# Performance work log

Hardware: AMD Instinct MI355X
Metric: run time of the kernel (lower is better)

## Reference

```python
import jax, jax.numpy as jnp
import numpy as np

N, G, E, R = 32768, 2048, 1146880, 3
NIN, GIN, F, OUT = 6, 4, 64, 1


def _w(k, fan_in, fan_out):
    return (jax.random.normal(k, (fan_in, fan_out), jnp.float32) / np.sqrt(fan_in)).astype(jnp.float32)


def setup_inputs() -> dict:
    key = jax.random.key(0)
    ks = jax.random.split(key, 20)
    x = jax.random.normal(ks[0], (N, NIN), jnp.float32)
    u = jax.random.normal(ks[1], (G, GIN), jnp.float32)
    batch = jnp.sort(jax.random.randint(ks[2], (N,), 0, G))
    hyperedge_index = jax.random.randint(ks[3], (R, E), 0, N)
    batch_hyper = jnp.sort(jax.random.randint(ks[4], (E,), 0, G))
    inp = {
        "x": x, "u": u, "batch": batch,
        "hyperedge_index": hyperedge_index, "batch_hyper": batch_hyper, "r": R,
        # mlp_x: (NIN+GIN)->F->F->F
        "W1": _w(ks[5], NIN + GIN, F), "b1": jnp.zeros((F,), jnp.float32),
        "W2": _w(ks[6], F, F), "b2": jnp.zeros((F,), jnp.float32),
        "W3": _w(ks[7], F, F), "b3": jnp.zeros((F,), jnp.float32),
        # weighting matrix [F,F]
        "weight": _w(ks[8], F, F),
        # x_hat: 2F->F->F->OUT
        "V1": _w(ks[9], 2 * F, F), "c1": jnp.zeros((F,), jnp.float32),
        "V2": _w(ks[10], F, F), "c2": jnp.zeros((F,), jnp.float32),
        "V3": _w(ks[11], F, OUT), "c3": jnp.zeros((OUT,), jnp.float32),
    }
    return inp


def _segment_softmax(x, idx, num_segments):
    # torch_geometric-style softmax grouped by idx along dim 0, per feature
    seg_max = jax.ops.segment_max(x, idx, num_segments=num_segments)
    ex = jnp.exp(x - seg_max[idx])
    denom = jax.ops.segment_sum(ex, idx, num_segments=num_segments)
    return ex / denom[idx]


def reference(x, u, batch, hyperedge_index, batch_hyper, r,
              W1, b1, W2, b2, W3, b3, weight, V1, c1, V2, c2, V3, c3):
    # mlp_x on [node_feats || global_feats_of_node's_graph]
    h = jnp.concatenate([x, u[batch]], axis=1)            # [N, NIN+GIN]
    h = jnp.maximum(h @ W1 + b1, 0.0)
    h = jnp.maximum(h @ W2 + b2, 0.0)
    h = h @ W3 + b3                                        # [N, F]

    # hyperedge finding: sum the r member-node embeddings of each hyperedge
    x_hyper = jnp.zeros((hyperedge_index.shape[1], h.shape[1]), h.dtype)
    for i in range(hyperedge_index.shape[0]):              # r is small & fixed
        x_hyper = x_hyper + jnp.take(h, hyperedge_index[i], axis=0)  # [E, F]

    # weighting: segment softmax over hyperedges of the same graph
    coef = _segment_softmax(x_hyper, batch_hyper, G)       # [E, F]
    x_hyper_hat = coef * jnp.maximum(x_hyper @ weight, 0.0)

    # x_hat head
    o = jnp.concatenate([x_hyper, x_hyper_hat], axis=1)    # [E, 2F]
    o = jnp.maximum(o @ V1 + c1, 0.0)
    o = jnp.maximum(o @ V2 + c2, 0.0)
    o = jax.nn.sigmoid(o @ V3 + c3)                        # [E, OUT]
    return (o, batch_hyper)
```

## Files before the change

### kernel.cpp

```cpp
#include <hip/hip_runtime.h>
#include <math.h>

typedef short bf16x8 __attribute__((ext_vector_type(8)));
typedef float f32x4  __attribute__((ext_vector_type(4)));
typedef unsigned short u16;
typedef unsigned int   u32;

#define MFMA16 __builtin_amdgcn_mfma_f32_16x16x32_bf16

__device__ __forceinline__ u16 f2b(float x) {
    union { float f; unsigned u; } v; v.f = x;
    unsigned r = v.u + 0x7fffu + ((v.u >> 16) & 1u);
    return (u16)(r >> 16);
}
__device__ __forceinline__ u16 f2bu(float x) {
    union { float f; unsigned u; } v; v.f = x;
    return (u16)((v.u + 0x8000u) >> 16);
}
__device__ __forceinline__ float b2f(u16 h) {
    union { unsigned u; float f; } v; v.u = ((unsigned)h) << 16;
    return v.f;
}
__device__ __forceinline__ float blo(u32 w) {
    union { u32 u; float f; } v; v.u = w << 16; return v.f;
}
__device__ __forceinline__ float bhi(u32 w) {
    union { u32 u; float f; } v; v.u = w & 0xffff0000u; return v.f;
}
__device__ __forceinline__ u32 add3pack(u32 x, u32 y, u32 z) {
    union { float f; u32 u; } lo, hi;
    lo.f = blo(x) + blo(y) + blo(z);
    hi.f = bhi(x) + bhi(y) + bhi(z);
    return __builtin_amdgcn_perm(hi.u + 0x8000u, lo.u + 0x8000u, 0x07060302u);
}

#define LOG2E 1.44269504088896340736f

__global__ __launch_bounds__(256) void prep_mlp_kernel(
    const float* __restrict__ x, const float* __restrict__ u,
    const int* __restrict__ batch,
    const float* __restrict__ W1, const float* __restrict__ b1,
    const float* __restrict__ W2, const float* __restrict__ b2,
    const float* __restrict__ W3, const float* __restrict__ b3,
    u16* __restrict__ hb, int N,
    const float* __restrict__ Wg, const float* __restrict__ V1g,
    const float* __restrict__ V2g, u16* __restrict__ SWZ,
    const int* __restrict__ bh, int E, int G, int* __restrict__ seg_start,
    int SB)
{
    const int b = blockIdx.x, tid = threadIdx.x;
    if (b < 32) {
        int idx = b * 256 + tid;
        int k = idx >> 6, n = idx & 63;
        int off = ((k >> 5) * 4 + (n >> 4)) * 640 + (n & 15) * 40 + ((k >> 3) & 3) * 8 + (k & 7);
        SWZ[5120 + off] = f2b(V1g[idx]);
        if (idx < 4096) {
            SWZ[off]         = f2b(Wg[idx]);
            SWZ[15360 + off] = f2b(V2g[idx]);
        }
        return;
    }
    if (b < 32 + SB) {
        int g = (b - 32) * 256 + tid;
        if (g > G) return;
        int lo = 0, hi = E;
        while (lo < hi) {
            int mid = (lo + hi) >> 1;
            if (bh[mid] < g) lo = mid + 1; else hi = mid;
        }
        seg_start[g] = lo;
        return;
    }
    __shared__ float inbuf[16][10];
    __shared__ float h1[16][64];
    __shared__ float h2[16][64];
    const int ni = tid >> 6, f = tid & 63;
    const int base = (b - 32 - SB) * 16;
    int nodes[4];
    #pragma unroll
    for (int s = 0; s < 4; ++s) {
        nodes[s] = min(base + s * 4 + ni, N - 1);
        if (f < 6)       inbuf[s * 4 + ni][f] = x[nodes[s] * 6 + f];
        else if (f < 10) inbuf[s * 4 + ni][f] = u[batch[nodes[s]] * 4 + (f - 6)];
    }
    __syncthreads();
    float acc[4];
    #pragma unroll
    for (int s = 0; s < 4; ++s) acc[s] = b1[f];
    #pragma unroll
    for (int k = 0; k < 10; ++k) {
        float w = W1[k * 64 + f];
        #pragma unroll
        for (int s = 0; s < 4; ++s) acc[s] = fmaf(inbuf[s * 4 + ni][k], w, acc[s]);
    }
    #pragma unroll
    for (int s = 0; s < 4; ++s) h1[s * 4 + ni][f] = fmaxf(acc[s], 0.f);
    __syncthreads();
    #pragma unroll
    for (int s = 0; s < 4; ++s) acc[s] = b2[f];
    #pragma unroll
    for (int k4 = 0; k4 < 16; ++k4) {
        float w0 = W2[(k4 * 4 + 0) * 64 + f];
        float w1 = W2[(k4 * 4 + 1) * 64 + f];
        float w2 = W2[(k4 * 4 + 2) * 64 + f];
        float w3 = W2[(k4 * 4 + 3) * 64 + f];
        #pragma unroll
        for (int s = 0; s < 4; ++s) {
            float4 hv = *(const float4*)&h1[s * 4 + ni][k4 * 4];
            acc[s] = fmaf(hv.x, w0, acc[s]);
            acc[s] = fmaf(hv.y, w1, acc[s]);
            acc[s] = fmaf(hv.z, w2, acc[s]);
            acc[s] = fmaf(hv.w, w3, acc[s]);
        }
    }
    #pragma unroll
    for (int s = 0; s < 4; ++s) h2[s * 4 + ni][f] = fmaxf(acc[s], 0.f);
    __syncthreads();
    #pragma unroll
    for (int s = 0; s < 4; ++s) acc[s] = b3[f];
    #pragma unroll
    for (int k4 = 0; k4 < 16; ++k4) {
        float w0 = W3[(k4 * 4 + 0) * 64 + f];
        float w1 = W3[(k4 * 4 + 1) * 64 + f];
        float w2 = W3[(k4 * 4 + 2) * 64 + f];
        float w3 = W3[(k4 * 4 + 3) * 64 + f];
        #pragma unroll
        for (int s = 0; s < 4; ++s) {
            float4 hv = *(const float4*)&h2[s * 4 + ni][k4 * 4];
            acc[s] = fmaf(hv.x, w0, acc[s]);
            acc[s] = fmaf(hv.y, w1, acc[s]);
            acc[s] = fmaf(hv.z, w2, acc[s]);
            acc[s] = fmaf(hv.w, w3, acc[s]);
        }
    }
    #pragma unroll
    for (int s = 0; s < 4; ++s) hb[nodes[s] * 64 + f] = f2b(acc[s]);
}

__global__ __launch_bounds__(256) void gather_stats_kernel(
    const u16* __restrict__ hb, const int* __restrict__ hidx,
    const int* __restrict__ seg_start,
    u16* __restrict__ Xh, float* __restrict__ Sinv,
    float* __restrict__ out, int E)
{
    __shared__ float ps[4][8][8];
    const int tid = threadIdx.x, lane = tid & 63, wid = tid >> 6;
    const int sub = lane >> 3, cl = lane & 7;
    const int g = blockIdx.x;
    const int e0 = seg_start[g], e1 = seg_start[g + 1];
    if (e1 <= e0) return;
    const int e1m1 = e1 - 1;
    const float gf = (float)g;

    for (int e = e0 + tid; e < e1; e += 256) out[E + e] = gf;

    float s[8] = {0.f, 0.f, 0.f, 0.f, 0.f, 0.f, 0.f, 0.f};
    for (int e = e0 + wid * 8 + sub; e < e1; e += 128) {
        #pragma unroll
        for (int j = 0; j < 4; ++j) {
            int ee = e + j * 32;
            int ec = min(ee, e1m1);
            int i0 = hidx[ec], i1 = hidx[E + ec], i2 = hidx[2 * E + ec];
            uint4 A0 = *(const uint4*)(hb + (size_t)i0 * 64 + cl * 8);
            uint4 A1 = *(const uint4*)(hb + (size_t)i1 * 64 + cl * 8);
            uint4 A2 = *(const uint4*)(hb + (size_t)i2 * 64 + cl * 8);
            u32 w0 = add3pack(A0.x, A1.x, A2.x);
            u32 w1 = add3pack(A0.y, A1.y, A2.y);
            u32 w2 = add3pack(A0.z, A1.z, A2.z);
            u32 w3 = add3pack(A0.w, A1.w, A2.w);
            if (ee < e1) {
                uint4 W; W.x = w0; W.y = w1; W.z = w2; W.w = w3;
                *(uint4*)(Xh + (size_t)ee * 64 + cl * 8) = W;
                s[0] += __expf(blo(w0)); s[1] += __expf(bhi(w0));
                s[2] += __expf(blo(w1)); s[3] += __expf(bhi(w1));
                s[4] += __expf(blo(w2)); s[5] += __expf(bhi(w2));
                s[6] += __expf(blo(w3)); s[7] += __expf(bhi(w3));
            }
        }
    }
    #pragma unroll
    for (int k = 0; k < 8; ++k) {
        s[k] += __shfl_xor(s[k], 8);
        s[k] += __shfl_xor(s[k], 16);
        s[k] += __shfl_xor(s[k], 32);
    }
    if (lane < 8) {
        #pragma unroll
        for (int k = 0; k < 8; ++k) ps[wid][lane][k] = s[k];
    }
    __syncthreads();
    if (tid < 64) {
        int c8 = tid >> 3, cc = tid & 7;
        float S = ps[0][c8][cc] + ps[1][c8][cc] + ps[2][c8][cc] + ps[3][c8][cc];
        Sinv[g * 64 + tid] = 1.f / S;
    }
}

__global__ __launch_bounds__(256, 3) void mfma_seg_kernel(
    const u16* __restrict__ Xh, const int* __restrict__ seg_start,
    const u16* __restrict__ SWZ, const float* __restrict__ Sinv,
    const float* __restrict__ c1g, const float* __restrict__ c2g,
    const float* __restrict__ V3g, const float* __restrict__ c3g,
    float* __restrict__ out, int E)
{
    __shared__ u16 SW[20480];
    __shared__ u16 XT_all[4][16 * 72];

    const int tid = threadIdx.x, lane = tid & 63, wid = tid >> 6;
    const int nl = lane & 15, rq = lane >> 4;
    const int g = blockIdx.x;
    const int e0 = seg_start[g], e1 = seg_start[g + 1];
    const int L = e1 - e0;
    if (L <= 0) return;
    const int e1m1 = e1 - 1;

    {
        const uint4* src = (const uint4*)SWZ;
        uint4* dst = (uint4*)SW;
        for (int i = tid; i < 2560; i += 256) dst[i] = src[i];
    }
    __syncthreads();
    const u16* WB  = SW;
    const u16* V1B = SW + 5120;
    const u16* V2B = SW + 15360;

    bf16x8 I0, I1;
    #pragma unroll
    for (int j = 0; j < 8; ++j) {
        I0[j] = (rq * 8 + j == nl)      ? (short)0x3F80 : (short)0;
        I1[j] = (rq * 8 + j == nl + 16) ? (short)0x3F80 : (short)0;
    }

    float l2d[4], c1v[4], c2v[4], v3v[4];
    #pragma unroll
    for (int nt = 0; nt < 4; ++nt) {
        int col = nt * 16 + nl;
        l2d[nt] = __log2f(Sinv[g * 64 + col]);
        c1v[nt] = c1g[col];
        c2v[nt] = c2g[col];
        v3v[nt] = V3g[col];
    }
    const float c3s = c3g[0];
    u16* XT = XT_all[wid];
    const f32x4 zf = {0.f, 0.f, 0.f, 0.f};

    auto loadA = [&](int tt, bf16x8& A0, bf16x8& A1) {
        const u16* xp = Xh + (size_t)min(e0 + tt * 16 + nl, e1m1) * 64 + rq * 8;
        A0 = *(const bf16x8*)(xp);
        A1 = *(const bf16x8*)(xp + 32);
    };

    int t = wid;
    bf16x8 p0 = {}, p1 = {};
    if (t * 16 < L) loadA(t, p0, p1);

    for (; t * 16 < L; t += 8) {
        const int eB1 = e0 + t * 16;
        const int eB2 = eB1 + 64;

        bf16x8 a0 = p0, a1 = p1;
        bf16x8 a2, a3;
        loadA(t + 4, a2, a3);
        if ((t + 8) * 16 < L) loadA(t + 8, p0, p1);

        f32x4 xc1[4], xc2[4];
        xc1[0] = MFMA16(a0, I0, zf, 0, 0, 0);
        xc1[1] = MFMA16(a0, I1, zf, 0, 0, 0);
        xc1[2] = MFMA16(a1, I0, zf, 0, 0, 0);
        xc1[3] = MFMA16(a1, I1, zf, 0, 0, 0);
        xc2[0] = MFMA16(a2, I0, zf, 0, 0, 0);
        xc2[1] = MFMA16(a2, I1, zf, 0, 0, 0);
        xc2[2] = MFMA16(a3, I0, zf, 0, 0, 0);
        xc2[3] = MFMA16(a3, I1, zf, 0, 0, 0);

        f32x4 acc1[4] = {zf, zf, zf, zf}, acc2t[4] = {zf, zf, zf, zf};
        #pragma unroll
        for (int nt = 0; nt < 4; ++nt) {
            bf16x8 b0 = *(const bf16x8*)(WB + (0 * 4 + nt) * 640 + nl * 40 + rq * 8);
            acc1[nt]  = MFMA16(a0, b0, acc1[nt], 0, 0, 0);
            acc2t[nt] = MFMA16(a2, b0, acc2t[nt], 0, 0, 0);
            bf16x8 b1 = *(const bf16x8*)(WB + (1 * 4 + nt) * 640 + nl * 40 + rq * 8);
            acc1[nt]  = MFMA16(a1, b1, acc1[nt], 0, 0, 0);
            acc2t[nt] = MFMA16(a3, b1, acc2t[nt], 0, 0, 0);
        }
        #pragma unroll
        for (int nt = 0; nt < 4; ++nt) {
            #pragma unroll
            for (int r = 0; r < 4; ++r) {
                float coef = __builtin_amdgcn_exp2f(
                    fmaf(xc1[nt][r], LOG2E, l2d[nt]));
                XT[(rq * 4 + r) * 72 + nt * 16 + nl] =
                    f2bu(coef * fmaxf(acc1[nt][r], 0.f));
            }
        }
        bf16x8 x2a = *(const bf16x8*)(XT + nl * 72 + rq * 8);
        bf16x8 x3a = *(const bf16x8*)(XT + nl * 72 + 32 + rq * 8);
        #pragma unroll
        for (int nt = 0; nt < 4; ++nt) {
            #pragma unroll
            for (int r = 0; r < 4; ++r) {
                float coef = __builtin_amdgcn_exp2f(
                    fmaf(xc2[nt][r], LOG2E, l2d[nt]));
                XT[(rq * 4 + r) * 72 + nt * 16 + nl] =
                    f2bu(coef * fmaxf(acc2t[nt][r], 0.f));
            }
        }
        bf16x8 x2b = *(const bf16x8*)(XT + nl * 72 + rq * 8);
        bf16x8 x3b = *(const bf16x8*)(XT + nl * 72 + 32 + rq * 8);

        f32x4 va[4], vb[4];
        #pragma unroll
        for (int nt = 0; nt < 4; ++nt) {
            va[nt][0] = c1v[nt]; va[nt][1] = c1v[nt];
            va[nt][2] = c1v[nt]; va[nt][3] = c1v[nt];
            vb[nt] = va[nt];
        }
        #pragma unroll
        for (int nt = 0; nt < 4; ++nt) {
            bf16x8 b0 = *(const bf16x8*)(V1B + (0 * 4 + nt) * 640 + nl * 40 + rq * 8);
            va[nt] = MFMA16(a0, b0, va[nt], 0, 0, 0);
            vb[nt] = MFMA16(a2, b0, vb[nt], 0, 0, 0);
            bf16x8 b1 = *(const bf16x8*)(V1B + (1 * 4 + nt) * 640 + nl * 40 + rq * 8);
            va[nt] = MFMA16(a1, b1, va[nt], 0, 0, 0);
            vb[nt] = MFMA16(a3, b1, vb[nt], 0, 0, 0);
        }
        #pragma unroll
        for (int nt = 0; nt < 4; ++nt) {
            bf16x8 b2 = *(const bf16x8*)(V1B + (2 * 4 + nt) * 640 + nl * 40 + rq * 8);
            va[nt] = MFMA16(x2a, b2, va[nt], 0, 0, 0);
            vb[nt] = MFMA16(x2b, b2, vb[nt], 0, 0, 0);
            bf16x8 b3 = *(const bf16x8*)(V1B + (3 * 4 + nt) * 640 + nl * 40 + rq * 8);
            va[nt] = MFMA16(x3a, b3, va[nt], 0, 0, 0);
            vb[nt] = MFMA16(x3b, b3, vb[nt], 0, 0, 0);
        }
        #pragma unroll
        for (int nt = 0; nt < 4; ++nt) {
            #pragma unroll
            for (int r = 0; r < 4; ++r)
                XT[(rq * 4 + r) * 72 + nt * 16 + nl] = f2bu(fmaxf(va[nt][r], 0.f));
        }
        bf16x8 o0a = *(const bf16x8*)(XT + nl * 72 + rq * 8);
        bf16x8 o1a = *(const bf16x8*)(XT + nl * 72 + 32 + rq * 8);
        #pragma unroll
        for (int nt = 0; nt < 4; ++nt) {
            #pragma unroll
            for (int r = 0; r < 4; ++r)
                XT[(rq * 4 + r) * 72 + nt * 16 + nl] = f2bu(fmaxf(vb[nt][r], 0.f));
        }
        bf16x8 o0b = *(const bf16x8*)(XT + nl * 72 + rq * 8);
        bf16x8 o1b = *(const bf16x8*)(XT + nl * 72 + 32 + rq * 8);

        f32x4 wa[4], wb2[4];
        #pragma unroll
        for (int nt = 0; nt < 4; ++nt) {
            wa[nt][0] = c2v[nt]; wa[nt][1] = c2v[nt];
            wa[nt][2] = c2v[nt]; wa[nt][3] = c2v[nt];
            wb2[nt] = wa[nt];
        }
        #pragma unroll
        for (int nt = 0; nt < 4; ++nt) {
            bf16x8 b0 = *(const bf16x8*)(V2B + (0 * 4 + nt) * 640 + nl * 40 + rq * 8);
            wa[nt]  = MFMA16(o0a, b0, wa[nt], 0, 0, 0);
            wb2[nt] = MFMA16(o0b, b0, wb2[nt], 0, 0, 0);
            bf16x8 b1 = *(const bf16x8*)(V2B + (1 * 4 + nt) * 640 + nl * 40 + rq * 8);
            wa[nt]  = MFMA16(o1a, b1, wa[nt], 0, 0, 0);
            wb2[nt] = MFMA16(o1b, b1, wb2[nt], 0, 0, 0);
        }

        float sra[4], srb[4];
        #pragma unroll
        for (int r = 0; r < 4; ++r) {
            float u1 = 0.f, u2 = 0.f;
            #pragma unroll
            for (int nt = 0; nt < 4; ++nt) {
                u1 = fmaf(fmaxf(wa[nt][r],  0.f), v3v[nt], u1);
                u2 = fmaf(fmaxf(wb2[nt][r], 0.f), v3v[nt], u2);
            }
            u1 += __shfl_xor(u1, 1); u2 += __shfl_xor(u2, 1);
            u1 += __shfl_xor(u1, 2); u2 += __shfl_xor(u2, 2);
            u1 += __shfl_xor(u1, 4); u2 += __shfl_xor(u2, 4);
            u1 += __shfl_xor(u1, 8); u2 += __shfl_xor(u2, 8);
            sra[r] = 1.f / (1.f + __expf(-(u1 + c3s)));
            srb[r] = 1.f / (1.f + __expf(-(u2 + c3s)));
        }
        if (nl == 0) {
            const int ra = eB1 + rq * 4;
            if (ra + 3 < e1) {
                *(float4*)(out + ra) = make_float4(sra[0], sra[1], sra[2], sra[3]);
            } else {
                #pragma unroll
                for (int r = 0; r < 4; ++r)
                    if (ra + r < e1) out[ra + r] = sra[r];
            }
            const int rb = eB2 + rq * 4;
            if (rb + 3 < e1) {
                *(float4*)(out + rb) = make_float4(srb[0], srb[1], srb[2], srb[3]);
            } else {
                #pragma unroll
                for (int r = 0; r < 4; ++r)
                    if (rb + r < e1) out[rb + r] = srb[r];
            }
        }
    }
}

extern "C" void kernel_launch(void* const* d_in, const int* in_sizes, int n_in,
                              void* d_out, int out_size, void* d_ws, size_t ws_size,
                              hipStream_t stream) {
    const float* x     = (const float*)d_in[0];
    const float* u     = (const float*)d_in[1];
    const int*   batch = (const int*)  d_in[2];
    const int*   hidx  = (const int*)  d_in[3];
    const int*   bh    = (const int*)  d_in[4];
    const float* W1 = (const float*)d_in[6];
    const float* b1 = (const float*)d_in[7];
    const float* W2 = (const float*)d_in[8];
    const float* b2 = (const float*)d_in[9];
    const float* W3 = (const float*)d_in[10];
    const float* b3 = (const float*)d_in[11];
    const float* Wg = (const float*)d_in[12];
    const float* V1 = (const float*)d_in[13];
    const float* c1 = (const float*)d_in[14];
    const float* V2 = (const float*)d_in[15];
    const float* c2 = (const float*)d_in[16];
    const float* V3 = (const float*)d_in[17];
    const float* c3 = (const float*)d_in[18];

    const int N = in_sizes[0] / 6;
    const int G = in_sizes[1] / 4;
    const int E = in_sizes[4];

    char* ws = (char*)d_ws;
    size_t off = 0;
    u16* hb = (u16*)(ws + off);            off += (size_t)N * 64 * 2;
    int* seg_start = (int*)(ws + off);     off += ((size_t)G + 1) * 4;
    off = (off + 255) & ~(size_t)255;
    u16* SWZ = (u16*)(ws + off);           off += 20480 * 2;
    float* Sinv = (float*)(ws + off);      off += (size_t)G * 64 * 4;
    off = (off + 255) & ~(size_t)255;
    u16* Xh = (u16*)(ws + off);            off += (size_t)E * 64 * 2;
    float* out = (float*)d_out;

    const int SB = (G + 256) / 256;
    const int NB = (N + 15) / 16;
    prep_mlp_kernel<<<32 + SB + NB, 256, 0, stream>>>(
        x, u, batch, W1, b1, W2, b2, W3, b3, hb, N,
        Wg, V1, V2, SWZ, bh, E, G, seg_start, SB);
    gather_stats_kernel<<<G, 256, 0, stream>>>(hb, hidx, seg_start, Xh, Sinv, out, E);
    mfma_seg_kernel<<<G, 256, 0, stream>>>(
        Xh, seg_start, SWZ, Sinv, c1, c2, V3, c3, out, E);
}
```

Baseline: 243.1 us.

## Repack intermediate tiles with XOR swizzle and packed stores, shrink LDS footprint

Removes the padded 40/72-stride layouts for the weight and transpose buffers in LDS. Each lane now writes four adjacent bf16 values as one packed 8-byte store into an XOR-swizzled 64-wide tile, replacing sixteen scalar 2-byte stores. To make this valid, the K dimension of V1 (second half) and V2 is permuted when the weights are pre-swizzled. The smaller LDS footprint allows launch bounds of 4 blocks per CU instead of 3, trading some register headroom for occupancy.

```diff
diff --git a/kernel.cpp b/kernel.cpp
--- a/kernel.cpp
+++ b/kernel.cpp
@@ -32,6 +32,11 @@
     lo.f = blo(x) + blo(y) + blo(z);
     hi.f = bhi(x) + bhi(y) + bhi(z);
     return __builtin_amdgcn_perm(hi.u + 0x8000u, lo.u + 0x8000u, 0x07060302u);
+}
+__device__ __forceinline__ u32 pack2(float lo, float hi) {
+    union { float f; u32 u; } a, b;
+    a.f = lo; b.f = hi;
+    return __builtin_amdgcn_perm(b.u + 0x8000u, a.u + 0x8000u, 0x07060302u);
 }
 
 #define LOG2E 1.44269504088896340736f
@@ -52,11 +57,15 @@
     if (b < 32) {
         int idx = b * 256 + tid;
         int k = idx >> 6, n = idx & 63;
-        int off = ((k >> 5) * 4 + (n >> 4)) * 640 + (n & 15) * 40 + ((k >> 3) & 3) * 8 + (k & 7);
-        SWZ[5120 + off] = f2b(V1g[idx]);
+        int s1 = (k < 64) ? k : (64 + (((k - 64) & 15) << 2) + ((k - 64) >> 4));
+        int off1 = ((s1 >> 5) * 4 + (n >> 4)) * 512 + (n & 15) * 32 + ((s1 >> 3) & 3) * 8 + (s1 & 7);
+        SWZ[4096 + off1] = f2b(V1g[idx]);
         if (idx < 4096) {
-            SWZ[off]         = f2b(Wg[idx]);
-            SWZ[15360 + off] = f2b(V2g[idx]);
+            int offw = ((k >> 5) * 4 + (n >> 4)) * 512 + (n & 15) * 32 + ((k >> 3) & 3) * 8 + (k & 7);
+            SWZ[offw] = f2b(Wg[idx]);
+            int s2 = ((k & 15) << 2) + (k >> 4);
+            int off2 = ((s2 >> 5) * 4 + (n >> 4)) * 512 + (n & 15) * 32 + ((s2 >> 3) & 3) * 8 + (s2 & 7);
+            SWZ[12288 + off2] = f2b(V2g[idx]);
         }
         return;
     }
@@ -196,15 +205,15 @@
     }
 }
 
-__global__ __launch_bounds__(256, 3) void mfma_seg_kernel(
+__global__ __launch_bounds__(256, 4) void mfma_seg_kernel(
     const u16* __restrict__ Xh, const int* __restrict__ seg_start,
     const u16* __restrict__ SWZ, const float* __restrict__ Sinv,
     const float* __restrict__ c1g, const float* __restrict__ c2g,
     const float* __restrict__ V3g, const float* __restrict__ c3g,
     float* __restrict__ out, int E)
 {
-    __shared__ u16 SW[20480];
-    __shared__ u16 XT_all[4][16 * 72];
+    __shared__ u16 SW[16384];
+    __shared__ u16 XT_all[4][16 * 64];
 
     const int tid = threadIdx.x, lane = tid & 63, wid = tid >> 6;
     const int nl = lane & 15, rq = lane >> 4;
@@ -217,12 +226,12 @@
     {
         const uint4* src = (const uint4*)SWZ;
         uint4* dst = (uint4*)SW;
-        for (int i = tid; i < 2560; i += 256) dst[i] = src[i];
+        for (int i = tid; i < 2048; i += 256) dst[i] = src[i];
     }
     __syncthreads();
     const u16* WB  = SW;
-    const u16* V1B = SW + 5120;
-    const u16* V2B = SW + 15360;
+    const u16* V1B = SW + 4096;
+    const u16* V2B = SW + 12288;
 
     bf16x8 I0, I1;
     #pragma unroll
@@ -243,6 +252,12 @@
     const float c3s = c3g[0];
     u16* XT = XT_all[wid];
     const f32x4 zf = {0.f, 0.f, 0.f, 0.f};
+
+    const int xw_swz = rq << 4;
+    const int xr_base = nl * 64;
+    const int xr_swz  = (nl & 12) << 2;
+    const int xr0 = xr_base + ((rq * 8) ^ xr_swz);
+    const int xr1 = xr_base + ((rq * 8 + 32) ^ xr_swz);
 
     auto loadA = [&](int tt, bf16x8& A0, bf16x8& A1) {
         const u16* xp = Xh + (size_t)min(e0 + tt * 16 + nl, e1m1) * 64 + rq * 8;
@@ -276,37 +291,35 @@
         f32x4 acc1[4] = {zf, zf, zf, zf}, acc2t[4] = {zf, zf, zf, zf};
         #pragma unroll
         for (int nt = 0; nt < 4; ++nt) {
-            bf16x8 b0 = *(const bf16x8*)(WB + (0 * 4 + nt) * 640 + nl * 40 + rq * 8);
+            bf16x8 b0 = *(const bf16x8*)(WB + (0 * 4 + nt) * 512 + nl * 32 + rq * 8);
             acc1[nt]  = MFMA16(a0, b0, acc1[nt], 0, 0, 0);
             acc2t[nt] = MFMA16(a2, b0, acc2t[nt], 0, 0, 0);
-            bf16x8 b1 = *(const bf16x8*)(WB + (1 * 4 + nt) * 640 + nl * 40 + rq * 8);
+            bf16x8 b1 = *(const bf16x8*)(WB + (1 * 4 + nt) * 512 + nl * 32 + rq * 8);
             acc1[nt]  = MFMA16(a1, b1, acc1[nt], 0, 0, 0);
             acc2t[nt] = MFMA16(a3, b1, acc2t[nt], 0, 0, 0);
         }
         #pragma unroll
-        for (int nt = 0; nt < 4; ++nt) {
-            #pragma unroll
-            for (int r = 0; r < 4; ++r) {
-                float coef = __builtin_amdgcn_exp2f(
-                    fmaf(xc1[nt][r], LOG2E, l2d[nt]));
-                XT[(rq * 4 + r) * 72 + nt * 16 + nl] =
-                    f2bu(coef * fmaxf(acc1[nt][r], 0.f));
-            }
-        }
-        bf16x8 x2a = *(const bf16x8*)(XT + nl * 72 + rq * 8);
-        bf16x8 x3a = *(const bf16x8*)(XT + nl * 72 + 32 + rq * 8);
-        #pragma unroll
-        for (int nt = 0; nt < 4; ++nt) {
-            #pragma unroll
-            for (int r = 0; r < 4; ++r) {
-                float coef = __builtin_amdgcn_exp2f(
-                    fmaf(xc2[nt][r], LOG2E, l2d[nt]));
-                XT[(rq * 4 + r) * 72 + nt * 16 + nl] =
-                    f2bu(coef * fmaxf(acc2t[nt][r], 0.f));
-            }
-        }
-        bf16x8 x2b = *(const bf16x8*)(XT + nl * 72 + rq * 8);
-        bf16x8 x3b = *(const bf16x8*)(XT + nl * 72 + 32 + rq * 8);
+        for (int r = 0; r < 4; ++r) {
+            float v0 = __builtin_amdgcn_exp2f(fmaf(xc1[0][r], LOG2E, l2d[0])) * fmaxf(acc1[0][r], 0.f);
+            float v1 = __builtin_amdgcn_exp2f(fmaf(xc1[1][r], LOG2E, l2d[1])) * fmaxf(acc1[1][r], 0.f);
+            float v2 = __builtin_amdgcn_exp2f(fmaf(xc1[2][r], LOG2E, l2d[2])) * fmaxf(acc1[2][r], 0.f);
+            float v3 = __builtin_amdgcn_exp2f(fmaf(xc1[3][r], LOG2E, l2d[3])) * fmaxf(acc1[3][r], 0.f);
+            uint2 w; w.x = pack2(v0, v1); w.y = pack2(v2, v3);
+            *(uint2*)(XT + (rq * 4 + r) * 64 + ((nl * 4) ^ xw_swz)) = w;
+        }
+        bf16x8 x2a = *(const bf16x8*)(XT + xr0);
+        bf16x8 x3a = *(const bf16x8*)(XT + xr1);
+        #pragma unroll
+        for (int r = 0; r < 4; ++r) {
+            float v0 = __builtin_amdgcn_exp2f(fmaf(xc2[0][r], LOG2E, l2d[0])) * fmaxf(acc2t[0][r], 0.f);
+            float v1 = __builtin_amdgcn_exp2f(fmaf(xc2[1][r], LOG2E, l2d[1])) * fmaxf(acc2t[1][r], 0.f);
+            float v2 = __builtin_amdgcn_exp2f(fmaf(xc2[2][r], LOG2E, l2d[2])) * fmaxf(acc2t[2][r], 0.f);
+            float v3 = __builtin_amdgcn_exp2f(fmaf(xc2[3][r], LOG2E, l2d[3])) * fmaxf(acc2t[3][r], 0.f);
+            uint2 w; w.x = pack2(v0, v1); w.y = pack2(v2, v3);
+            *(uint2*)(XT + (rq * 4 + r) * 64 + ((nl * 4) ^ xw_swz)) = w;
+        }
+        bf16x8 x2b = *(const bf16x8*)(XT + xr0);
+        bf16x8 x3b = *(const bf16x8*)(XT + xr1);
 
         f32x4 va[4], vb[4];
         #pragma unroll
@@ -317,38 +330,40 @@
         }
         #pragma unroll
         for (int nt = 0; nt < 4; ++nt) {
-            bf16x8 b0 = *(const bf16x8*)(V1B + (0 * 4 + nt) * 640 + nl * 40 + rq * 8);
+            bf16x8 b0 = *(const bf16x8*)(V1B + (0 * 4 + nt) * 512 + nl * 32 + rq * 8);
             va[nt] = MFMA16(a0, b0, va[nt], 0, 0, 0);
             vb[nt] = MFMA16(a2, b0, vb[nt], 0, 0, 0);
-            bf16x8 b1 = *(const bf16x8*)(V1B + (1 * 4 + nt) * 640 + nl * 40 + rq * 8);
+            bf16x8 b1 = *(const bf16x8*)(V1B + (1 * 4 + nt) * 512 + nl * 32 + rq * 8);
             va[nt] = MFMA16(a1, b1, va[nt], 0, 0, 0);
             vb[nt] = MFMA16(a3, b1, vb[nt], 0, 0, 0);
         }
         #pragma unroll
         for (int nt = 0; nt < 4; ++nt) {
-            bf16x8 b2 = *(const bf16x8*)(V1B + (2 * 4 + nt) * 640 + nl * 40 + rq * 8);
+            bf16x8 b2 = *(const bf16x8*)(V1B + (2 * 4 + nt) * 512 + nl * 32 + rq * 8);
             va[nt] = MFMA16(x2a, b2, va[nt], 0, 0, 0);
             vb[nt] = MFMA16(x2b, b2, vb[nt], 0, 0, 0);
-            bf16x8 b3 = *(const bf16x8*)(V1B + (3 * 4 + nt) * 640 + nl * 40 + rq * 8);
+            bf16x8 b3 = *(const bf16x8*)(V1B + (3 * 4 + nt) * 512 + nl * 32 + rq * 8);
             va[nt] = MFMA16(x3a, b3, va[nt], 0, 0, 0);
             vb[nt] = MFMA16(x3b, b3, vb[nt], 0, 0, 0);
         }
         #pragma unroll
-        for (int nt = 0; nt < 4; ++nt) {
-            #pragma unroll
-            for (int r = 0; r < 4; ++r)
-                XT[(rq * 4 + r) * 72 + nt * 16 + nl] = f2bu(fmaxf(va[nt][r], 0.f));
-        }
-        bf16x8 o0a = *(const bf16x8*)(XT + nl * 72 + rq * 8);
-        bf16x8 o1a = *(const bf16x8*)(XT + nl * 72 + 32 + rq * 8);
-        #pragma unroll
-        for (int nt = 0; nt < 4; ++nt) {
-            #pragma unroll
-            for (int r = 0; r < 4; ++r)
-                XT[(rq * 4 + r) * 72 + nt * 16 + nl] = f2bu(fmaxf(vb[nt][r], 0.f));
-        }
-        bf16x8 o0b = *(const bf16x8*)(XT + nl * 72 + rq * 8);
-        bf16x8 o1b = *(const bf16x8*)(XT + nl * 72 + 32 + rq * 8);
+        for (int r = 0; r < 4; ++r) {
+            uint2 w;
+            w.x = pack2(fmaxf(va[0][r], 0.f), fmaxf(va[1][r], 0.f));
+            w.y = pack2(fmaxf(va[2][r], 0.f), fmaxf(va[3][r], 0.f));
+            *(uint2*)(XT + (rq * 4 + r) * 64 + ((nl * 4) ^ xw_swz)) = w;
+        }
+        bf16x8 o0a = *(const bf16x8*)(XT + xr0);
+        bf16x8 o1a = *(const bf16x8*)(XT + xr1);
+        #pragma unroll
+        for (int r = 0; r < 4; ++r) {
+            uint2 w;
+            w.x = pack2(fmaxf(vb[0][r], 0.f), fmaxf(vb[1][r], 0.f));
+            w.y = pack2(fmaxf(vb[2][r], 0.f), fmaxf(vb[3][r], 0.f));
+            *(uint2*)(XT + (rq * 4 + r) * 64 + ((nl * 4) ^ xw_swz)) = w;
+        }
+        bf16x8 o0b = *(const bf16x8*)(XT + xr0);
+        bf16x8 o1b = *(const bf16x8*)(XT + xr1);
 
         f32x4 wa[4], wb2[4];
         #pragma unroll
@@ -359,10 +374,10 @@
         }
         #pragma unroll
         for (int nt = 0; nt < 4; ++nt) {
-            bf16x8 b0 = *(const bf16x8*)(V2B + (0 * 4 + nt) * 640 + nl * 40 + rq * 8);
+            bf16x8 b0 = *(const bf16x8*)(V2B + (0 * 4 + nt) * 512 + nl * 32 + rq * 8);
             wa[nt]  = MFMA16(o0a, b0, wa[nt], 0, 0, 0);
             wb2[nt] = MFMA16(o0b, b0, wb2[nt], 0, 0, 0);
-            bf16x8 b1 = *(const bf16x8*)(V2B + (1 * 4 + nt) * 640 + nl * 40 + rq * 8);
+            bf16x8 b1 = *(const bf16x8*)(V2B + (1 * 4 + nt) * 512 + nl * 32 + rq * 8);
             wa[nt]  = MFMA16(o1a, b1, wa[nt], 0, 0, 0);
             wb2[nt] = MFMA16(o1b, b1, wb2[nt], 0, 0, 0);
         }
@@ -435,7 +450,7 @@
     u16* hb = (u16*)(ws + off);            off += (size_t)N * 64 * 2;
     int* seg_start = (int*)(ws + off);     off += ((size_t)G + 1) * 4;
     off = (off + 255) & ~(size_t)255;
-    u16* SWZ = (u16*)(ws + off);           off += 20480 * 2;
+    u16* SWZ = (u16*)(ws + off);           off += 16384 * 2;
     float* Sinv = (float*)(ws + off);      off += (size_t)G * 64 * 4;
     off = (off + 255) & ~(size_t)255;
     u16* Xh = (u16*)(ws + off);            off += (size_t)E * 64 * 2;
```

After: 244.3 us. Within noise of the previous version (+0.5%).
